# Performance work log

Hardware: AMD Instinct MI355X
Metric: run time of the kernel (lower is better)

The kernel has to match this reference:

```python
import jax, jax.numpy as jnp
import numpy as np

EMBED = 768
HEADS = 12
HEAD_DIM = EMBED // HEADS
RATES = (1, 2, 4)
SEGS = (2048, 4096, 8192)


def setup_inputs() -> dict:
    key = jax.random.key(0)
    k1, k2, k3 = jax.random.split(key, 3)
    b, n = 2, 8192
    x = jax.random.normal(k1, (b, n, EMBED), dtype=jnp.float32)
    Wqkv = jax.random.normal(k2, (3 * EMBED, EMBED), dtype=jnp.float32) * 0.02
    Wout = jax.random.normal(k3, (EMBED, EMBED), dtype=jnp.float32) * 0.02
    return {"x": x, "Wqkv": Wqkv, "Wout": Wout}


def _dilated_attention(qkv):
    # qkv: [b, n, 3, h, d]
    b, n, _, h, d = qkv.shape
    scale = 1.0 / jnp.sqrt(jnp.asarray(d, qkv.dtype))
    out = jnp.zeros((b, n, h, d), dtype=qkv.dtype)
    for r, s in zip(RATES, SEGS):
        sr = s // r
        nseg = n // s
        # strided gather: [b, nseg, sr, 3, h, d]
        g = qkv.reshape(b, nseg, s, 3, h, d)[:, :, ::r]
        # fold stride offset into batch; attention runs over the segment axis
        g = g.transpose(0, 2, 1, 3, 4, 5).reshape(b * sr, nseg, 3, h, d)
        q, k, v = g[:, :, 0], g[:, :, 1], g[:, :, 2]
        scores = jnp.einsum('bnhd,bmhd->bhnm', q, k) * scale
        attn = jax.nn.softmax(scores, axis=-1)
        o = jnp.einsum('bhnm,bmhd->bnhd', attn, v)
        # scatter-add back into strided positions
        o = o.reshape(b, sr, nseg, h, d).transpose(0, 2, 1, 3, 4)
        out = out.reshape(b, nseg, s, h, d).at[:, :, ::r].add(o).reshape(b, n, h, d)
    # normalize over full sequence dim (as in original module)
    out = out / out.sum(axis=1, keepdims=True)
    return out


def reference(x, Wqkv, Wout):
    b, n, e = x.shape
    qkv = (x @ Wqkv.T).reshape(b, n, 3, HEADS, HEAD_DIM)
    o = _dilated_attention(qkv)  # [b, n, h, d]
    return o.reshape(b, n, e) @ Wout.T
```

## Files before the change

### kernel.cpp

```cpp
#include <hip/hip_runtime.h>

typedef unsigned short u16;
typedef __attribute__((ext_vector_type(8))) short bf16x8;
typedef __attribute__((ext_vector_type(4))) float f32x4;

__device__ __forceinline__ u16 f2bf_rne(float f) {
  unsigned u = __float_as_uint(f);
  u += 0x7fffu + ((u >> 16) & 1u);
  return (u16)(u >> 16);
}
__device__ __forceinline__ float bf2f(u16 h) {
  return __uint_as_float(((unsigned)h) << 16);
}
__device__ __forceinline__ void split1(float v, u16& h, u16& l) {
  u16 hh = f2bf_rne(v);
  h = hh;
  l = f2bf_rne(v - bf2f(hh));
}

__device__ __forceinline__ void gl16(const void* g, void* l) {
  __builtin_amdgcn_global_load_lds(
      (const __attribute__((address_space(1))) unsigned int*)g,
      (__attribute__((address_space(3))) unsigned int*)l,
      16, 0, 0);
}

__global__ void split_convert_all(const float4* __restrict__ x,
                                  ushort4* __restrict__ xhi, ushort4* __restrict__ xlo,
                                  const float4* __restrict__ wq,
                                  ushort4* __restrict__ wqh, ushort4* __restrict__ wql) {
  int i = blockIdx.x * 256 + threadIdx.x;
  const float4* src;
  ushort4 *dh, *dl;
  int idx;
  if (i < 3145728) { src = x; dh = xhi; dl = xlo; idx = i; }
  else if (i < 3588096) { src = wq; dh = wqh; dl = wql; idx = i - 3145728; }
  else return;
  float4 v = src[idx];
  ushort4 h, l;
  split1(v.x, h.x, l.x); split1(v.y, h.y, l.y);
  split1(v.z, h.z, l.z); split1(v.w, h.w, l.w);
  dh[idx] = h; dl[idx] = l;
}

__global__ __launch_bounds__(256, 2) void gemm_split_bt(
    const u16* __restrict__ Ahi, const u16* __restrict__ Alo, int lda,
    const u16* __restrict__ Bhi, const u16* __restrict__ Blo,
    const u16* __restrict__ Bhi2, const u16* __restrict__ Blo2,
    float* __restrict__ C, int M, int N, int K) {
  __shared__ __align__(16) u16 sAh[2][4096], sAl[2][4096];
  __shared__ __align__(16) u16 sBh[2][4096], sBl[2][4096];
  const int tid = threadIdx.x;
  const int wave = tid >> 6;
  const int lane = tid & 63;
  const int tm0 = blockIdx.x * 128;
  const int tn0 = blockIdx.y * 128;
  const int wm = (wave & 1) * 64;
  const int wn = (wave >> 1) * 64;
  if (2 * tm0 >= M) { Bhi = Bhi2; Blo = Blo2; }

  const int r4 = lane >> 2;
  const int sc = ((lane & 3) ^ ((r4 >> 1) & 3)) * 8;
  const int srow = wave * 32 + r4;
  const u16* gAh = Ahi + (size_t)(tm0 + srow) * lda + sc;
  const u16* gAl = Alo + (size_t)(tm0 + srow) * lda + sc;
  const u16* gBh = Bhi + (size_t)(tn0 + srow) * K + sc;
  const u16* gBl = Blo + (size_t)(tn0 + srow) * K + sc;
  const size_t rA = (size_t)16 * lda;
  const size_t rB = (size_t)16 * K;
  const int ldst = wave * 1024;

  auto stage = [&](int t, int b) {
    const int kk = t << 5;
    gl16(gAh + kk, &sAh[b][ldst]);
    gl16(gAh + kk + rA, &sAh[b][ldst + 512]);
    gl16(gAl + kk, &sAl[b][ldst]);
    gl16(gAl + kk + rA, &sAl[b][ldst + 512]);
    gl16(gBh + kk, &sBh[b][ldst]);
    gl16(gBh + kk + rB, &sBh[b][ldst + 512]);
    gl16(gBl + kk, &sBl[b][ldst]);
    gl16(gBl + kk + rB, &sBl[b][ldst + 512]);
  };

  f32x4 acc[4][4] = {};
  const int fr = lane & 15;
  const int quad = lane >> 4;
  const int k0 = (quad ^ ((fr >> 1) & 3)) * 8;
  const int nt = K >> 5;

  stage(0, 0);
  __syncthreads();

  for (int t = 0; t < nt; ++t) {
    const int cb = t & 1;
    if (t + 1 < nt) stage(t + 1, cb ^ 1);
    bf16x8 ah[4], al[4], bh[4], bl[4];
#pragma unroll
    for (int i = 0; i < 4; ++i) {
      ah[i] = *(const bf16x8*)&sAh[cb][(wm + i * 16 + fr) * 32 + k0];
      al[i] = *(const bf16x8*)&sAl[cb][(wm + i * 16 + fr) * 32 + k0];
      bh[i] = *(const bf16x8*)&sBh[cb][(wn + i * 16 + fr) * 32 + k0];
      bl[i] = *(const bf16x8*)&sBl[cb][(wn + i * 16 + fr) * 32 + k0];
    }
#pragma unroll
    for (int i = 0; i < 4; ++i)
#pragma unroll
      for (int j = 0; j < 4; ++j) {
        acc[i][j] = __builtin_amdgcn_mfma_f32_16x16x32_bf16(ah[i], bh[j], acc[i][j], 0, 0, 0);
        acc[i][j] = __builtin_amdgcn_mfma_f32_16x16x32_bf16(ah[i], bl[j], acc[i][j], 0, 0, 0);
        acc[i][j] = __builtin_amdgcn_mfma_f32_16x16x32_bf16(al[i], bh[j], acc[i][j], 0, 0, 0);
      }
    __syncthreads();
  }

  const int col = lane & 15;
  const int rowq = (lane >> 4) * 4;
#pragma unroll
  for (int i = 0; i < 4; ++i)
#pragma unroll
    for (int j = 0; j < 4; ++j) {
      size_t base = (size_t)(tm0 + wm + i * 16 + rowq) * N + (tn0 + wn + j * 16 + col);
#pragma unroll
      for (int r = 0; r < 4; ++r) C[base + (size_t)r * N] = acc[i][j][r];
    }
}

__global__ __launch_bounds__(256) void attn_dilated(const float* __restrict__ qkv,
                                                    u16* __restrict__ qk16,
                                                    float* __restrict__ Spart) {
  __shared__ float rows[4][2312];
  __shared__ float sc[12][16];
  __shared__ float Aw[12][16];
  const int t = threadIdx.x;
  const int i0 = blockIdx.x;
  const int b = blockIdx.y;
  const size_t rowbase = (size_t)b * 8192 + i0;

  for (int idx = t; idx < 4 * 576; idx += 256) {
    int j = idx / 576, c4 = idx - j * 576;
    ((float4*)rows[j])[c4] = ((const float4*)(qkv + (rowbase + 2048 * j) * 2304))[c4];
  }
  __syncthreads();

  if (t < 192) {
    int h = t >> 4, j = (t >> 2) & 3, jp = t & 3;
    const float4* q = (const float4*)&rows[j][h * 64];
    const float4* k = (const float4*)&rows[jp][768 + h * 64];
    float s = 0.f;
#pragma unroll
    for (int d = 0; d < 16; ++d) {
      float4 a = q[d], bb = k[d];
      s += a.x * bb.x + a.y * bb.y + a.z * bb.z + a.w * bb.w;
    }
    sc[h][(j << 2) | jp] = s * 0.125f;
  }
  __syncthreads();

  if (t < 48) {
    int h = t >> 2, j = t & 3;
    float s0 = sc[h][j * 4 + 0], s1 = sc[h][j * 4 + 1];
    float s2 = sc[h][j * 4 + 2], s3 = sc[h][j * 4 + 3];
    float m = fmaxf(fmaxf(s0, s1), fmaxf(s2, s3));
    float e0 = expf(s0 - m), e1 = expf(s1 - m), e2 = expf(s2 - m), e3 = expf(s3 - m);
    float inv = 1.f / (e0 + e1 + e2 + e3);
    float a[4] = {e0 * inv, e1 * inv, e2 * inv, e3 * inv};
    if ((i0 & 1) == 0) {
      int p = j ^ 2;
      float ss = sc[h][j * 4 + j], sx = sc[h][j * 4 + p];
      float mm = fmaxf(ss, sx);
      float es = expf(ss - mm), ex = expf(sx - mm);
      float iv = 1.f / (es + ex);
      a[j] += es * iv;
      a[p] += ex * iv;
    }
    if ((i0 & 3) == 0) a[j] += 1.f;
    Aw[h][j * 4 + 0] = a[0]; Aw[h][j * 4 + 1] = a[1];
    Aw[h][j * 4 + 2] = a[2]; Aw[h][j * 4 + 3] = a[3];
  }
  __syncthreads();

  float* sp = Spart + ((size_t)b * 64 + (i0 & 63)) * 768;
#pragma unroll
  for (int rep = 0; rep < 3; ++rep) {
    int cc = rep * 256 + t;
    int h = cc >> 6;
    float ps = 0.f;
#pragma unroll
    for (int j = 0; j < 4; ++j) {
      float v = 0.f;
#pragma unroll
      for (int jp = 0; jp < 4; ++jp) v = fmaf(Aw[h][(j << 2) | jp], rows[jp][1536 + cc], v);
      u16 h16, l16;
      split1(v, h16, l16);
      size_t base = (rowbase + 2048 * j) * 4608;
      qk16[base + cc] = h16;
      qk16[base + 768 + cc] = l16;
      ps += v;
    }
    atomicAdd(&sp[cc], ps);
  }
}

__global__ void colred(const float* __restrict__ Spart, float* __restrict__ Sinv) {
  int i = blockIdx.x * 256 + threadIdx.x;
  if (i >= 1536) return;
  int b = i / 768, c = i - b * 768;
  const float* p = Spart + (size_t)b * 64 * 768 + c;
  float s = 0.f;
#pragma unroll
  for (int g = 0; g < 64; ++g) s += p[g * 768];
  Sinv[i] = 1.0f / s;
}

__global__ void scale_wout(const float4* __restrict__ Wout, const float* __restrict__ Sinv,
                           ushort4* __restrict__ wh0, ushort4* __restrict__ wl0,
                           ushort4* __restrict__ wh1, ushort4* __restrict__ wl1) {
  int i = blockIdx.x * 256 + threadIdx.x;
  if (i >= 294912) return;
  int b = i / 147456;
  int r = i - b * 147456;
  int c = (r % 192) * 4;
  const float* s = Sinv + b * 768 + c;
  float4 v = Wout[r];
  v.x *= s[0]; v.y *= s[1]; v.z *= s[2]; v.w *= s[3];
  ushort4 h, l;
  split1(v.x, h.x, l.x); split1(v.y, h.y, l.y);
  split1(v.z, h.z, l.z); split1(v.w, h.w, l.w);
  if (b == 0) { wh0[r] = h; wl0[r] = l; }
  else        { wh1[r] = h; wl1[r] = l; }
}

extern "C" void kernel_launch(void* const* d_in, const int* in_sizes, int n_in,
                              void* d_out, int out_size, void* d_ws, size_t ws_size,
                              hipStream_t stream) {
  (void)in_sizes; (void)n_in; (void)out_size; (void)ws_size;
  const float* x = (const float*)d_in[0];
  const float* Wqkv = (const float*)d_in[1];
  const float* Wout = (const float*)d_in[2];
  float* out = (float*)d_out;

  char* w = (char*)d_ws;
  float* qkv = (float*)(w);
  u16* qk16 = (u16*)(w);
  size_t off = 150994944;
  u16* xhi = (u16*)(w + off);
  float* Spart = (float*)(w + off);
  float* Sinv = (float*)(w + off + 393216);
  u16* wh0 = (u16*)(w + off + 400000);
  u16* wl0 = (u16*)(w + off + 1579648);
  u16* wh1 = (u16*)(w + off + 2759296);
  u16* wl1 = (u16*)(w + off + 3938944);
  off += 25165824;
  u16* xlo = (u16*)(w + off); off += 25165824;
  u16* wqh = (u16*)(w + off); off += 3538944;
  u16* wql = (u16*)(w + off); off += 3538944;

  split_convert_all<<<dim3(14016), 256, 0, stream>>>(
      (const float4*)x, (ushort4*)xhi, (ushort4*)xlo,
      (const float4*)Wqkv, (ushort4*)wqh, (ushort4*)wql);

  gemm_split_bt<<<dim3(128, 18), 256, 0, stream>>>(xhi, xlo, 768, wqh, wql, wqh, wql,
                                                   qkv, 16384, 2304, 768);

  hipMemsetAsync(Spart, 0, 393216, stream);
  attn_dilated<<<dim3(2048, 2), 256, 0, stream>>>(qkv, qk16, Spart);

  colred<<<dim3(6), 256, 0, stream>>>(Spart, Sinv);

  scale_wout<<<dim3(1152), 256, 0, stream>>>((const float4*)Wout, Sinv,
                                             (ushort4*)wh0, (ushort4*)wl0,
                                             (ushort4*)wh1, (ushort4*)wl1);

  gemm_split_bt<<<dim3(128, 6), 256, 0, stream>>>(qk16, qk16 + 768, 4608,
                                                  wh0, wl0, wh1, wl1,
                                                  out, 16384, 768, 768);
}
```

Before: 400.8 us.

## Remove LDS double buffering in split GEMM and raise occupancy bound

The split-bf16 GEMM now uses a single LDS buffer per operand instead of double buffering. Each K-step loads, syncs, then computes, and launch bounds move from 2 to 4 blocks per CU. The aim is to hide memory latency with more resident blocks rather than in-block prefetch. The risks are losing load/compute overlap within each block and register pressure or spills under the tighter bound.

```diff
diff --git a/kernel.cpp b/kernel.cpp
--- a/kernel.cpp
+++ b/kernel.cpp
@@ -43,13 +43,12 @@
   dh[idx] = h; dl[idx] = l;
 }
 
-__global__ __launch_bounds__(256, 2) void gemm_split_bt(
+__global__ __launch_bounds__(256, 4) void gemm_split_bt(
     const u16* __restrict__ Ahi, const u16* __restrict__ Alo, int lda,
     const u16* __restrict__ Bhi, const u16* __restrict__ Blo,
     const u16* __restrict__ Bhi2, const u16* __restrict__ Blo2,
     float* __restrict__ C, int M, int N, int K) {
-  __shared__ __align__(16) u16 sAh[2][4096], sAl[2][4096];
-  __shared__ __align__(16) u16 sBh[2][4096], sBl[2][4096];
+  __shared__ __align__(16) u16 sAh[4096], sAl[4096], sBh[4096], sBl[4096];
   const int tid = threadIdx.x;
   const int wave = tid >> 6;
   const int lane = tid & 63;
@@ -70,37 +69,28 @@
   const size_t rB = (size_t)16 * K;
   const int ldst = wave * 1024;
 
-  auto stage = [&](int t, int b) {
-    const int kk = t << 5;
-    gl16(gAh + kk, &sAh[b][ldst]);
-    gl16(gAh + kk + rA, &sAh[b][ldst + 512]);
-    gl16(gAl + kk, &sAl[b][ldst]);
-    gl16(gAl + kk + rA, &sAl[b][ldst + 512]);
-    gl16(gBh + kk, &sBh[b][ldst]);
-    gl16(gBh + kk + rB, &sBh[b][ldst + 512]);
-    gl16(gBl + kk, &sBl[b][ldst]);
-    gl16(gBl + kk + rB, &sBl[b][ldst + 512]);
-  };
-
   f32x4 acc[4][4] = {};
   const int fr = lane & 15;
   const int quad = lane >> 4;
   const int k0 = (quad ^ ((fr >> 1) & 3)) * 8;
-  const int nt = K >> 5;
-
-  stage(0, 0);
-  __syncthreads();
-
-  for (int t = 0; t < nt; ++t) {
-    const int cb = t & 1;
-    if (t + 1 < nt) stage(t + 1, cb ^ 1);
+
+  for (int kt = 0; kt < K; kt += 32) {
+    gl16(gAh + kt, &sAh[ldst]);
+    gl16(gAh + kt + rA, &sAh[ldst + 512]);
+    gl16(gAl + kt, &sAl[ldst]);
+    gl16(gAl + kt + rA, &sAl[ldst + 512]);
+    gl16(gBh + kt, &sBh[ldst]);
+    gl16(gBh + kt + rB, &sBh[ldst + 512]);
+    gl16(gBl + kt, &sBl[ldst]);
+    gl16(gBl + kt + rB, &sBl[ldst + 512]);
+    __syncthreads();
     bf16x8 ah[4], al[4], bh[4], bl[4];
 #pragma unroll
     for (int i = 0; i < 4; ++i) {
-      ah[i] = *(const bf16x8*)&sAh[cb][(wm + i * 16 + fr) * 32 + k0];
-      al[i] = *(const bf16x8*)&sAl[cb][(wm + i * 16 + fr) * 32 + k0];
-      bh[i] = *(const bf16x8*)&sBh[cb][(wn + i * 16 + fr) * 32 + k0];
-      bl[i] = *(const bf16x8*)&sBl[cb][(wn + i * 16 + fr) * 32 + k0];
+      ah[i] = *(const bf16x8*)&sAh[(wm + i * 16 + fr) * 32 + k0];
+      al[i] = *(const bf16x8*)&sAl[(wm + i * 16 + fr) * 32 + k0];
+      bh[i] = *(const bf16x8*)&sBh[(wn + i * 16 + fr) * 32 + k0];
+      bl[i] = *(const bf16x8*)&sBl[(wn + i * 16 + fr) * 32 + k0];
     }
 #pragma unroll
     for (int i = 0; i < 4; ++i)
```

After: 383.8 us. 4.2% less time.
